# Kernel optimization log

Hardware: AMD Instinct MI355X
Metric: run time of the kernel (lower is better)

Reference implementation:

```python
import jax, jax.numpy as jnp
import numpy as np

NEG_SLOPE = 0.2  # PyG GATConv default negative_slope


def _gat_layer(x, src, dst, W, a_s, a_d, b, heads, ch):
    N = x.shape[0]
    h = (x @ W).reshape(N, heads, ch)                      # [N,H,C]
    al_s = jnp.sum(h * a_s[None], axis=-1)                 # [N,H]
    al_d = jnp.sum(h * a_d[None], axis=-1)                 # [N,H]
    e = jax.nn.leaky_relu(al_s[src] + al_d[dst], NEG_SLOPE)  # [E,H]
    m = jax.ops.segment_max(e, dst, num_segments=N)        # segment-softmax (stable)
    ex = jnp.exp(e - jax.lax.stop_gradient(m)[dst])
    denom = jax.ops.segment_sum(ex, dst, num_segments=N)
    alpha = ex / (denom[dst] + 1e-16)                      # [E,H]
    msg = h[src] * alpha[..., None]                        # [E,H,C]
    out = jax.ops.segment_sum(msg, dst, num_segments=N)    # [N,H,C]
    return out.reshape(N, heads * ch) + b


def _add_self_loops(edge_index, N):
    loop = jnp.arange(N, dtype=edge_index.dtype)
    src = jnp.concatenate([edge_index[0], loop])
    dst = jnp.concatenate([edge_index[1], loop])
    return src, dst


def gat_forward(x, edge_index, batch, W1, a_src1, a_dst1, b1, W2, a_src2, a_dst2, b2, W3, a_src3, a_dst3, b3, num_graphs=512):
    N = x.shape[0]
    src, dst = _add_self_loops(edge_index, N)
    x = jax.nn.relu(_gat_layer(x, src, dst, W1, a_src1, a_dst1, b1, 4, 64))
    x = jax.nn.relu(_gat_layer(x, src, dst, W2, a_src2, a_dst2, b2, 4, 64))
    x = _gat_layer(x, src, dst, W3, a_src3, a_dst3, b3, 1, 32)
    # global_mean_pool
    sums = jax.ops.segment_sum(x, batch, num_segments=num_graphs)
    cnt = jax.ops.segment_sum(jnp.ones((N,), x.dtype), batch, num_segments=num_graphs)
    return sums / jnp.maximum(cnt, 1.0)[:, None]


def setup_inputs() -> dict:
    key = jax.random.key(0)
    ks = jax.random.split(key, 16)
    N, E, G = 50000, 800000, 512
    IN, HID, H, OUT = 775, 64, 4, 32
    s = 0.05
    return {
        "x": jax.random.normal(ks[0], (N, IN), jnp.float32),
        "edge_index": jax.random.randint(ks[1], (2, E), 0, N, jnp.int32),
        "batch": jnp.sort(jax.random.randint(ks[2], (N,), 0, G, jnp.int32)),
        "W1": jax.random.normal(ks[3], (IN, H * HID), jnp.float32) * s,
        "a_src1": jax.random.normal(ks[4], (H, HID), jnp.float32) * s,
        "a_dst1": jax.random.normal(ks[5], (H, HID), jnp.float32) * s,
        "b1": jnp.zeros((H * HID,), jnp.float32),
        "W2": jax.random.normal(ks[6], (H * HID, H * HID), jnp.float32) * s,
        "a_src2": jax.random.normal(ks[7], (H, HID), jnp.float32) * s,
        "a_dst2": jax.random.normal(ks[8], (H, HID), jnp.float32) * s,
        "b2": jnp.zeros((H * HID,), jnp.float32),
        "W3": jax.random.normal(ks[9], (H * HID, OUT), jnp.float32) * s,
        "a_src3": jax.random.normal(ks[10], (1, OUT), jnp.float32) * s,
        "a_dst3": jax.random.normal(ks[11], (1, OUT), jnp.float32) * s,
        "b3": jnp.zeros((OUT,), jnp.float32),
    }


def reference(x, edge_index, batch, W1, a_src1, a_dst1, b1, W2, a_src2, a_dst2, b2, W3, a_src3, a_dst3, b3):
    return gat_forward(x, edge_index, batch, W1, a_src1, a_dst1, b1, W2, a_src2, a_dst2, b2, W3, a_src3, a_dst3, b3)
```

## Files before the change

### kernel.cpp

```cpp
#include <hip/hip_runtime.h>
#include <hip/hip_bf16.h>

typedef unsigned short u16;
typedef __attribute__((ext_vector_type(4))) unsigned short u16x4;
typedef __attribute__((ext_vector_type(8))) unsigned short u16x8;
typedef __attribute__((ext_vector_type(8))) short bf16x8;
typedef __attribute__((ext_vector_type(4))) float f32x4;

__device__ __forceinline__ u16 f2bs(float f) {
    union { float f; unsigned int u; } x; x.f = f;
    unsigned int r = x.u + 0x7FFFu + ((x.u >> 16) & 1u);
    return (u16)(r >> 16);
}
__device__ __forceinline__ float bs2f(u16 u) {
    union { unsigned int u; float f; } x; x.u = ((unsigned int)u) << 16; return x.f;
}
__device__ __forceinline__ float lrelu(float e) { return e >= 0.f ? e : 0.2f * e; }

__global__ void deg_kernel(const int* __restrict__ dst, int* __restrict__ deg, int E) {
    int i = blockIdx.x * 256 + threadIdx.x;
    if (i < E) atomicAdd(&deg[dst[i]], 1);
}

__global__ __launch_bounds__(1024) void scan_local(const int* __restrict__ deg,
        int* __restrict__ ptr, int* __restrict__ bsum, int N) {
    __shared__ int wsum[16];
    const int t = threadIdx.x, i = blockIdx.x * 1024 + t;
    const int lane = t & 63, w = t >> 6;
    int v = (i < N) ? deg[i] : 0;
    int x = v;
    #pragma unroll
    for (int off = 1; off < 64; off <<= 1) { int y = __shfl_up(x, off); if (lane >= off) x += y; }
    if (lane == 63) wsum[w] = x;
    __syncthreads();
    if (w == 0) {
        int s = (lane < 16) ? wsum[lane] : 0;
        #pragma unroll
        for (int off = 1; off < 16; off <<= 1) { int y = __shfl_up(s, off); if (lane >= off) s += y; }
        if (lane < 16) wsum[lane] = s;
    }
    __syncthreads();
    int incl = x + (w > 0 ? wsum[w - 1] : 0);
    if (i < N) ptr[i + 1] = incl;
    if (t == 0) bsum[blockIdx.x] = wsum[15];
}

__global__ __launch_bounds__(64) void scan_carry(int* __restrict__ bsum, int nb) {
    int t = threadIdx.x;
    int v = (t < nb) ? bsum[t] : 0;
    int x = v;
    #pragma unroll
    for (int off = 1; off < 64; off <<= 1) { int y = __shfl_up(x, off); if (t >= off) x += y; }
    if (t < nb) bsum[t] = x - v;
}

__global__ __launch_bounds__(1024) void scan_final(const int* __restrict__ deg,
        int* __restrict__ ptr, int* __restrict__ cur, const int* __restrict__ bsum, int N) {
    int i = blockIdx.x * 1024 + threadIdx.x;
    if (i == 0) ptr[0] = 0;
    if (i < N) {
        int p = ptr[i + 1] + bsum[blockIdx.x];
        ptr[i + 1] = p;
        cur[i] = p - deg[i];
    }
}

__global__ void fill_kernel(const int* __restrict__ src, const int* __restrict__ dst,
        int* __restrict__ cur, int* __restrict__ csr, int E) {
    int i = blockIdx.x * 256 + threadIdx.x;
    if (i < E) { int p = atomicAdd(&cur[dst[i]], 1); csr[p] = src[i]; }
}

__global__ void bounds_kernel(const int* __restrict__ batch, int* __restrict__ gstart,
        int N, int G) {
    int i = blockIdx.x * 256 + threadIdx.x;
    if (i > N) return;
    if (i == 0) {
        int b0 = batch[0];
        for (int g = 0; g <= b0; g++) gstart[g] = 0;
    } else if (i == N) {
        int bl = batch[N - 1];
        for (int g = bl + 1; g <= G; g++) gstart[g] = N;
    } else {
        int b = batch[i], bp = batch[i - 1];
        for (int g = bp + 1; g <= b; g++) gstart[g] = i;
    }
}

__global__ void transpose_w(const float* __restrict__ W, u16* __restrict__ Wt,
        int K, int Nn, int KT) {
    int idx = blockIdx.x * 256 + threadIdx.x;
    if (idx >= Nn * KT) return;
    int n = idx / KT, k = idx - n * KT;
    Wt[(size_t)n * KT + k] = (k < K) ? f2bs(W[(size_t)k * Nn + n]) : (u16)0;
}

__global__ __launch_bounds__(256) void conv_x(const float* __restrict__ x,
        u16* __restrict__ xbf, int N) {
    const int idx = blockIdx.x * 256 + threadIdx.x;
    if (idx >= N * 200) return;
    const int r = idx / 200;
    const int k4 = (idx - r * 200) * 4;
    const float* row = x + (size_t)r * 775;
    u16x4 o;
    #pragma unroll
    for (int u = 0; u < 4; u++) {
        const int k = k4 + u;
        o[u] = (k < 775) ? f2bs(row[k]) : (u16)0;
    }
    *(u16x4*)&xbf[(size_t)r * 800 + k4] = o;
}

template<bool AFP32>
__global__ __launch_bounds__(256) void gemm128(
        const void* __restrict__ Av, int lda, int M, int K,
        const u16* __restrict__ B, int ldb,
        u16* __restrict__ C, int ldc) {
    const float* Af = (const float*)Av;
    const u16*   Au = (const u16*)Av;
    __shared__ u16 Alds[128][40];
    __shared__ u16 Blds[128][40];
    const int t = threadIdx.x;
    const int row0 = blockIdx.x * 128, col0 = blockIdx.y * 128;
    const int wid = t >> 6, lane = t & 63;
    const int wm = wid >> 1, wn = wid & 1;
    const int quad = lane >> 4, l16 = lane & 15;

    f32x4 acc[4][4];
    f32x4 z = {0.f, 0.f, 0.f, 0.f};
    #pragma unroll
    for (int i = 0; i < 4; i++)
        #pragma unroll
        for (int j = 0; j < 4; j++) acc[i][j] = z;

    const int kTiles = (K + 31) >> 5;
    for (int kt = 0; kt < kTiles; ++kt) {
        const int k0 = kt << 5;
        #pragma unroll
        for (int c = 0; c < 2; c++) {
            int ch = t + c * 256;
            int r = ch >> 2, cp = (ch & 3) * 8;
            int gr = row0 + r;
            u16x8 v = {0,0,0,0,0,0,0,0};
            if (AFP32) {
                #pragma unroll
                for (int u = 0; u < 8; u++) {
                    int k = k0 + cp + u;
                    v[u] = (gr < M && k < K) ? f2bs(Af[(size_t)gr * lda + k]) : (u16)0;
                }
            } else {
                if (gr < M) v = *(const u16x8*)(Au + (size_t)gr * lda + k0 + cp);
            }
            *(u16x8*)&Alds[r][cp] = v;
        }
        #pragma unroll
        for (int c = 0; c < 2; c++) {
            int ch = t + c * 256;
            int r = ch >> 2, cp = (ch & 3) * 8;
            *(u16x8*)&Blds[r][cp] = *(const u16x8*)(B + (size_t)(col0 + r) * ldb + k0 + cp);
        }
        __syncthreads();
        bf16x8 af[4], bfr[4];
        #pragma unroll
        for (int it = 0; it < 4; it++) af[it] = *(const bf16x8*)&Alds[wm * 64 + it * 16 + l16][quad * 8];
        #pragma unroll
        for (int jt = 0; jt < 4; jt++) bfr[jt] = *(const bf16x8*)&Blds[wn * 64 + jt * 16 + l16][quad * 8];
        #pragma unroll
        for (int it = 0; it < 4; it++)
            #pragma unroll
            for (int jt = 0; jt < 4; jt++)
                acc[it][jt] = __builtin_amdgcn_mfma_f32_16x16x32_bf16(af[it], bfr[jt], acc[it][jt], 0, 0, 0);
        __syncthreads();
    }
    #pragma unroll
    for (int it = 0; it < 4; it++) {
        int gr0 = row0 + wm * 64 + it * 16 + quad * 4;
        #pragma unroll
        for (int jt = 0; jt < 4; jt++) {
            int gc = col0 + wn * 64 + jt * 16 + l16;
            #pragma unroll
            for (int r = 0; r < 4; r++) {
                int gr = gr0 + r;
                if (gr < M) C[(size_t)gr * ldc + gc] = f2bs(acc[it][jt][r]);
            }
        }
    }
}

__global__ __launch_bounds__(256) void gemm32(
        const u16* __restrict__ A, int lda, int M, int K,
        const u16* __restrict__ B, int ldb, float* __restrict__ C) {
    __shared__ u16 Alds[128][40];
    __shared__ u16 Blds[32][40];
    const int t = threadIdx.x;
    const int row0 = blockIdx.x * 128;
    const int wid = t >> 6, lane = t & 63;
    const int quad = lane >> 4, l16 = lane & 15;
    f32x4 acc[2][2];
    f32x4 z = {0.f, 0.f, 0.f, 0.f};
    acc[0][0] = z; acc[0][1] = z; acc[1][0] = z; acc[1][1] = z;
    const int kTiles = K >> 5;
    for (int kt = 0; kt < kTiles; ++kt) {
        const int k0 = kt << 5;
        #pragma unroll
        for (int c = 0; c < 2; c++) {
            int ch = t + c * 256;
            int r = ch >> 2, cp = (ch & 3) * 8;
            int gr = row0 + r;
            u16x8 v = {0,0,0,0,0,0,0,0};
            if (gr < M) v = *(const u16x8*)(A + (size_t)gr * lda + k0 + cp);
            *(u16x8*)&Alds[r][cp] = v;
        }
        if (t < 128) {
            int r = t >> 2, cp = (t & 3) * 8;
            *(u16x8*)&Blds[r][cp] = *(const u16x8*)(B + (size_t)r * ldb + k0 + cp);
        }
        __syncthreads();
        bf16x8 af[2], bfr[2];
        #pragma unroll
        for (int it = 0; it < 2; it++) af[it] = *(const bf16x8*)&Alds[wid * 32 + it * 16 + l16][quad * 8];
        #pragma unroll
        for (int jt = 0; jt < 2; jt++) bfr[jt] = *(const bf16x8*)&Blds[jt * 16 + l16][quad * 8];
        #pragma unroll
        for (int it = 0; it < 2; it++)
            #pragma unroll
            for (int jt = 0; jt < 2; jt++)
                acc[it][jt] = __builtin_amdgcn_mfma_f32_16x16x32_bf16(af[it], bfr[jt], acc[it][jt], 0, 0, 0);
        __syncthreads();
    }
    #pragma unroll
    for (int it = 0; it < 2; it++) {
        int gr0 = row0 + wid * 32 + it * 16 + quad * 4;
        #pragma unroll
        for (int jt = 0; jt < 2; jt++) {
            int gc = jt * 16 + l16;
            #pragma unroll
            for (int r = 0; r < 4; r++) {
                int gr = gr0 + r;
                if (gr < M) C[(size_t)gr * 32 + gc] = acc[it][jt][r];
            }
        }
    }
}

__global__ __launch_bounds__(256) void al_kernel(const u16* __restrict__ h,
        const float* __restrict__ a_s, const float* __restrict__ a_d,
        float* __restrict__ als, float* __restrict__ ald, int N) {
    const int t = threadIdx.x, wid = t >> 6, lane = t & 63;
    const f32x4 as4 = *(const f32x4*)&a_s[lane * 4];
    const f32x4 ad4 = *(const f32x4*)&a_d[lane * 4];
    #pragma unroll
    for (int u = 0; u < 2; u++) {
        const int n = blockIdx.x * 8 + wid * 2 + u;
        if (n >= N) return;
        const u16x4 hv = *(const u16x4*)&h[(size_t)n * 256 + lane * 4];
        float ps = 0.f, pd = 0.f;
        #pragma unroll
        for (int c = 0; c < 4; c++) {
            const float f = bs2f(hv[c]);
            ps = fmaf(f, as4[c], ps);
            pd = fmaf(f, ad4[c], pd);
        }
        #pragma unroll
        for (int off = 8; off >= 1; off >>= 1) {
            ps += __shfl_xor(ps, off, 16);
            pd += __shfl_xor(pd, off, 16);
        }
        if ((lane & 15) == 0) {
            als[n * 4 + (lane >> 4)] = ps;
            ald[n * 4 + (lane >> 4)] = pd;
        }
    }
}

__global__ __launch_bounds__(256) void al3_kernel(const float* __restrict__ h3,
        const float* __restrict__ a_s, const float* __restrict__ a_d,
        float* __restrict__ als, float* __restrict__ ald, int N) {
    int t = threadIdx.x, wid = t >> 6, lane = t & 63;
    int c = lane & 31, half = lane >> 5;
    float as = a_s[c], ad = a_d[c];
    int n = blockIdx.x * 8 + wid * 2 + half;
    if (n >= N) return;
    float hv = h3[(size_t)n * 32 + c];
    float ps = hv * as, pd = hv * ad;
    for (int off = 16; off >= 1; off >>= 1) { ps += __shfl_down(ps, off, 32); pd += __shfl_down(pd, off, 32); }
    if (c == 0) { als[n] = ps; ald[n] = pd; }
}

__global__ __launch_bounds__(256) void agg_kernel(const u16* __restrict__ hbuf,
        const float* __restrict__ als, const float* __restrict__ ald,
        const int* __restrict__ ptr, const int* __restrict__ csr,
        const float* __restrict__ bias, u16* __restrict__ act, int N) {
    __shared__ float al_lds[4][64][4];
    __shared__ int   s_lds[4][64];
    const int t = threadIdx.x, wid = t >> 6, lane = t & 63;
    const int i = blockIdx.x * 4 + wid;
    if (i >= N) return;
    const int start = ptr[i], end = ptr[i + 1];
    const int deg = end - start;
    const int col8 = lane & 31;
    const int half = lane >> 5;
    const int head8 = col8 >> 3;

    const f32x4 aldv = *(const f32x4*)&ald[(size_t)i * 4];
    const f32x4 alsv = *(const f32x4*)&als[(size_t)i * 4];
    f32x4 eself;
    #pragma unroll
    for (int hh = 0; hh < 4; hh++) eself[hh] = lrelu(alsv[hh] + aldv[hh]);

    float acc[8];
    f32x4 mx, inv;

    if (deg <= 64) {
        int sreg = 0;
        f32x4 ev;
        #pragma unroll
        for (int hh = 0; hh < 4; hh++) ev[hh] = -1e30f;
        if (lane < deg) {
            sreg = csr[start + lane];
            const f32x4 a = *(const f32x4*)&als[(size_t)sreg * 4];
            #pragma unroll
            for (int hh = 0; hh < 4; hh++) ev[hh] = lrelu(a[hh] + aldv[hh]);
        }
        #pragma unroll
        for (int hh = 0; hh < 4; hh++) mx[hh] = fmaxf(eself[hh], ev[hh]);
        #pragma unroll
        for (int off = 32; off >= 1; off >>= 1) {
            #pragma unroll
            for (int hh = 0; hh < 4; hh++) mx[hh] = fmaxf(mx[hh], __shfl_xor(mx[hh], off));
        }
        f32x4 sm, av;
        #pragma unroll
        for (int hh = 0; hh < 4; hh++) {
            av[hh] = (lane < deg) ? expf(ev[hh] - mx[hh]) : 0.f;
            sm[hh] = av[hh] + ((lane == 0) ? expf(eself[hh] - mx[hh]) : 0.f);
        }
        #pragma unroll
        for (int off = 32; off >= 1; off >>= 1) {
            #pragma unroll
            for (int hh = 0; hh < 4; hh++) sm[hh] += __shfl_xor(sm[hh], off);
        }
        #pragma unroll
        for (int hh = 0; hh < 4; hh++) inv[hh] = 1.f / (sm[hh] + 1e-16f);
        #pragma unroll
        for (int hh = 0; hh < 4; hh++) av[hh] *= inv[hh];
        *(f32x4*)&al_lds[wid][lane][0] = av;
        s_lds[wid][lane] = sreg;

        const u16x8 hrs = *(const u16x8*)&hbuf[(size_t)i * 256 + col8 * 8];
        const float aself = expf(eself[head8] - mx[head8]) * inv[head8];
        #pragma unroll
        for (int c = 0; c < 8; c++) acc[c] = (half == 0) ? aself * bs2f(hrs[c]) : 0.f;

        int k = half;
        for (; k + 6 < deg; k += 8) {
            const int s0 = s_lds[wid][k],     s1 = s_lds[wid][k + 2];
            const int s2 = s_lds[wid][k + 4], s3 = s_lds[wid][k + 6];
            const float a0 = al_lds[wid][k][head8],     a1 = al_lds[wid][k + 2][head8];
            const float a2 = al_lds[wid][k + 4][head8], a3 = al_lds[wid][k + 6][head8];
            const u16x8 h0 = *(const u16x8*)&hbuf[(size_t)s0 * 256 + col8 * 8];
            const u16x8 h1 = *(const u16x8*)&hbuf[(size_t)s1 * 256 + col8 * 8];
            const u16x8 h2 = *(const u16x8*)&hbuf[(size_t)s2 * 256 + col8 * 8];
            const u16x8 h3v = *(const u16x8*)&hbuf[(size_t)s3 * 256 + col8 * 8];
            #pragma unroll
            for (int c = 0; c < 8; c++) {
                acc[c] = fmaf(a0, bs2f(h0[c]), acc[c]);
                acc[c] = fmaf(a1, bs2f(h1[c]), acc[c]);
                acc[c] = fmaf(a2, bs2f(h2[c]), acc[c]);
                acc[c] = fmaf(a3, bs2f(h3v[c]), acc[c]);
            }
        }
        for (; k < deg; k += 2) {
            const int s = s_lds[wid][k];
            const float a = al_lds[wid][k][head8];
            const u16x8 hr = *(const u16x8*)&hbuf[(size_t)s * 256 + col8 * 8];
            #pragma unroll
            for (int c = 0; c < 8; c++) acc[c] = fmaf(a, bs2f(hr[c]), acc[c]);
        }
    } else {
        mx = eself;
        for (int j = start + lane; j < end; j += 64) {
            int s = csr[j];
            const f32x4 a = *(const f32x4*)&als[(size_t)s * 4];
            #pragma unroll
            for (int hh = 0; hh < 4; hh++) mx[hh] = fmaxf(mx[hh], lrelu(a[hh] + aldv[hh]));
        }
        #pragma unroll
        for (int off = 32; off >= 1; off >>= 1) {
            #pragma unroll
            for (int hh = 0; hh < 4; hh++) mx[hh] = fmaxf(mx[hh], __shfl_xor(mx[hh], off));
        }
        f32x4 sm;
        #pragma unroll
        for (int hh = 0; hh < 4; hh++) sm[hh] = (lane == 0) ? expf(eself[hh] - mx[hh]) : 0.f;
        for (int j = start + lane; j < end; j += 64) {
            int s = csr[j];
            const f32x4 a = *(const f32x4*)&als[(size_t)s * 4];
            #pragma unroll
            for (int hh = 0; hh < 4; hh++) sm[hh] += expf(lrelu(a[hh] + aldv[hh]) - mx[hh]);
        }
        #pragma unroll
        for (int off = 32; off >= 1; off >>= 1) {
            #pragma unroll
            for (int hh = 0; hh < 4; hh++) sm[hh] += __shfl_xor(sm[hh], off);
        }
        #pragma unroll
        for (int hh = 0; hh < 4; hh++) inv[hh] = 1.f / (sm[hh] + 1e-16f);

        const u16x8 hrs = *(const u16x8*)&hbuf[(size_t)i * 256 + col8 * 8];
        const float aself = expf(eself[head8] - mx[head8]) * inv[head8];
        #pragma unroll
        for (int c = 0; c < 8; c++) acc[c] = (half == 0) ? aself * bs2f(hrs[c]) : 0.f;

        for (int base = start; base < end; base += 64) {
            const int n64 = min(64, end - base);
            const int j = base + lane;
            int sreg = 0;
            if (j < end) {
                sreg = csr[j];
                const f32x4 a = *(const f32x4*)&als[(size_t)sreg * 4];
                f32x4 alpha;
                #pragma unroll
                for (int hh = 0; hh < 4; hh++)
                    alpha[hh] = expf(lrelu(a[hh] + aldv[hh]) - mx[hh]) * inv[hh];
                *(f32x4*)&al_lds[wid][lane][0] = alpha;
            }
            s_lds[wid][lane] = sreg;
            for (int k = half; k < n64; k += 2) {
                const int s = s_lds[wid][k];
                const float a = al_lds[wid][k][head8];
                const u16x8 hr = *(const u16x8*)&hbuf[(size_t)s * 256 + col8 * 8];
                #pragma unroll
                for (int c = 0; c < 8; c++) acc[c] = fmaf(a, bs2f(hr[c]), acc[c]);
            }
        }
    }

    #pragma unroll
    for (int c = 0; c < 8; c++) acc[c] += __shfl_down(acc[c], 32);
    if (half == 0) {
        const f32x4 bv0 = *(const f32x4*)&bias[col8 * 8];
        const f32x4 bv1 = *(const f32x4*)&bias[col8 * 8 + 4];
        u16x8 o;
        #pragma unroll
        for (int c = 0; c < 4; c++) o[c] = f2bs(fmaxf(acc[c] + bv0[c], 0.f));
        #pragma unroll
        for (int c = 4; c < 8; c++) o[c] = f2bs(fmaxf(acc[c] + bv1[c - 4], 0.f));
        *(u16x8*)&act[(size_t)i * 256 + col8 * 8] = o;
    }
}

__global__ __launch_bounds__(256) void agg3_kernel(const float* __restrict__ h3,
        const float* __restrict__ als, const float* __restrict__ ald,
        const int* __restrict__ ptr, const int* __restrict__ csr,
        const float* __restrict__ bias, float* __restrict__ out_n, int N) {
    __shared__ float a_lds[4][64];
    __shared__ int   s_lds3[4][64];
    const int t = threadIdx.x, wid = t >> 6, lane = t & 63;
    const int col = lane & 31, half = lane >> 5;
    const int i = blockIdx.x * 4 + wid;
    if (i >= N) return;
    const int start = ptr[i], end = ptr[i + 1];
    const int deg = end - start;
    const float aldv = ald[i];
    const float e0 = lrelu(als[i] + aldv);
    float acc = 0.f;

    if (deg <= 64) {
        int sreg = 0; float ev = -1e30f;
        if (lane < deg) { sreg = csr[start + lane]; ev = lrelu(als[sreg] + aldv); }
        float mx = fmaxf(e0, ev);
        #pragma unroll
        for (int off = 32; off >= 1; off >>= 1) mx = fmaxf(mx, __shfl_xor(mx, off));
        float ex = (lane < deg) ? expf(ev - mx) : 0.f;
        float sm = ex + ((lane == 0) ? expf(e0 - mx) : 0.f);
        #pragma unroll
        for (int off = 32; off >= 1; off >>= 1) sm += __shfl_xor(sm, off);
        const float inv = 1.f / (sm + 1e-16f);
        a_lds[wid][lane] = ex * inv;
        s_lds3[wid][lane] = sreg;
        if (half == 0) acc = expf(e0 - mx) * inv * h3[(size_t)i * 32 + col];

        int k = half;
        for (; k + 6 < deg; k += 8) {
            const int s0 = s_lds3[wid][k],     s1 = s_lds3[wid][k + 2];
            const int s2 = s_lds3[wid][k + 4], s3 = s_lds3[wid][k + 6];
            const float a0 = a_lds[wid][k],     a1 = a_lds[wid][k + 2];
            const float a2 = a_lds[wid][k + 4], a3 = a_lds[wid][k + 6];
            const float v0 = h3[(size_t)s0 * 32 + col];
            const float v1 = h3[(size_t)s1 * 32 + col];
            const float v2 = h3[(size_t)s2 * 32 + col];
            const float v3 = h3[(size_t)s3 * 32 + col];
            acc = fmaf(a0, v0, acc); acc = fmaf(a1, v1, acc);
            acc = fmaf(a2, v2, acc); acc = fmaf(a3, v3, acc);
        }
        for (; k < deg; k += 2)
            acc = fmaf(a_lds[wid][k], h3[(size_t)s_lds3[wid][k] * 32 + col], acc);
    } else {
        float mx = e0;
        for (int j = start + lane; j < end; j += 64)
            mx = fmaxf(mx, lrelu(als[csr[j]] + aldv));
        #pragma unroll
        for (int off = 32; off >= 1; off >>= 1) mx = fmaxf(mx, __shfl_xor(mx, off));
        float sm = (lane == 0) ? expf(e0 - mx) : 0.f;
        for (int j = start + lane; j < end; j += 64)
            sm += expf(lrelu(als[csr[j]] + aldv) - mx);
        #pragma unroll
        for (int off = 32; off >= 1; off >>= 1) sm += __shfl_xor(sm, off);
        const float inv = 1.f / (sm + 1e-16f);
        if (half == 0) acc = expf(e0 - mx) * inv * h3[(size_t)i * 32 + col];
        for (int base = start; base < end; base += 64) {
            const int n64 = min(64, end - base);
            const int j = base + lane;
            int sreg = 0; float av = 0.f;
            if (j < end) {
                sreg = csr[j];
                av = expf(lrelu(als[sreg] + aldv) - mx) * inv;
            }
            a_lds[wid][lane] = av;
            s_lds3[wid][lane] = sreg;
            for (int k = half; k < n64; k += 2)
                acc = fmaf(a_lds[wid][k], h3[(size_t)s_lds3[wid][k] * 32 + col], acc);
        }
    }

    acc += __shfl_down(acc, 32);
    if (half == 0)
        out_n[(size_t)i * 32 + col] = acc + bias[col];
}

__global__ __launch_bounds__(256) void pool_kernel(const float* __restrict__ out_n,
        const int* __restrict__ gstart, float* __restrict__ out, int G) {
    const int t = threadIdx.x, wid = t >> 6, lane = t & 63;
    const int col = lane & 31, half = lane >> 5;
    const int g = blockIdx.x * 4 + wid;
    if (g >= G) return;
    const int s = gstart[g], e = gstart[g + 1];
    float acc = 0.f;
    int r = s + half;
    for (; r + 6 < e; r += 8) {
        acc += out_n[(size_t)r * 32 + col];
        acc += out_n[(size_t)(r + 2) * 32 + col];
        acc += out_n[(size_t)(r + 4) * 32 + col];
        acc += out_n[(size_t)(r + 6) * 32 + col];
    }
    for (; r < e; r += 2) acc += out_n[(size_t)r * 32 + col];
    acc += __shfl_down(acc, 32);
    if (half == 0)
        out[g * 32 + col] = acc / fmaxf((float)(e - s), 1.f);
}

extern "C" void kernel_launch(void* const* d_in, const int* in_sizes, int n_in,
                              void* d_out, int out_size, void* d_ws, size_t ws_size,
                              hipStream_t stream) {
    const int N = 50000, E = 800000, G = 512;
    const float* x    = (const float*)d_in[0];
    const int*   ei   = (const int*)d_in[1];
    const int*   batch= (const int*)d_in[2];
    const float* W1   = (const float*)d_in[3];
    const float* as1  = (const float*)d_in[4];
    const float* ad1  = (const float*)d_in[5];
    const float* b1   = (const float*)d_in[6];
    const float* W2   = (const float*)d_in[7];
    const float* as2  = (const float*)d_in[8];
    const float* ad2  = (const float*)d_in[9];
    const float* b2   = (const float*)d_in[10];
    const float* W3   = (const float*)d_in[11];
    const float* as3  = (const float*)d_in[12];
    const float* ad3  = (const float*)d_in[13];
    const float* b3   = (const float*)d_in[14];
    const int* esrc = ei;
    const int* edst = ei + E;

    char* base = (char*)d_ws; size_t off = 0;
    auto alloc = [&](size_t bytes) -> void* {
        void* p = base + off; off = (off + bytes + 255) & ~(size_t)255; return p;
    };
    u16*   hbuf = (u16*)  alloc((size_t)N * 256 * 2);
    u16*   act  = (u16*)  alloc((size_t)N * 256 * 2);
    float* h3   = (float*)alloc((size_t)N * 32 * 4);
    float* als  = (float*)alloc((size_t)N * 4 * 4);
    float* ald  = (float*)alloc((size_t)N * 4 * 4);
    int*   deg  = (int*)  alloc((size_t)N * 4);
    int*   ptr  = (int*)  alloc((size_t)(N + 1) * 4);
    int*   cur  = (int*)  alloc((size_t)N * 4);
    int*   csr  = (int*)  alloc((size_t)E * 4);
    u16*   Wt   = (u16*)  alloc((size_t)256 * 800 * 2);
    int*   bsum = (int*)  alloc((size_t)64 * 4);
    float* out_n= (float*)alloc((size_t)N * 32 * 4);
    int*   gstart=(int*)  alloc((size_t)(G + 1) * 4);
    u16*   xbf  = (u16*)  alloc((size_t)N * 800 * 2);
    const bool use_xbf = (off <= ws_size);

    hipMemsetAsync(deg, 0, (size_t)N * 4, stream);

    const int nb = (N + 1023) / 1024;
    deg_kernel<<<(E + 255) / 256, 256, 0, stream>>>(edst, deg, E);
    scan_local<<<nb, 1024, 0, stream>>>(deg, ptr, bsum, N);
    scan_carry<<<1, 64, 0, stream>>>(bsum, nb);
    scan_final<<<nb, 1024, 0, stream>>>(deg, ptr, cur, bsum, N);
    fill_kernel<<<(E + 255) / 256, 256, 0, stream>>>(esrc, edst, cur, csr, E);
    bounds_kernel<<<(N + 256) / 256, 256, 0, stream>>>(batch, gstart, N, G);

    dim3 g128((N + 127) / 128, 2);
    const int aggGrid = (N + 3) / 4;
    transpose_w<<<(256 * 800 + 255) / 256, 256, 0, stream>>>(W1, Wt, 775, 256, 800);
    if (use_xbf) {
        conv_x<<<(N * 200 + 255) / 256, 256, 0, stream>>>(x, xbf, N);
        gemm128<false><<<g128, 256, 0, stream>>>(xbf, 800, N, 775, Wt, 800, hbuf, 256);
    } else {
        gemm128<true><<<g128, 256, 0, stream>>>(x, 775, N, 775, Wt, 800, hbuf, 256);
    }
    al_kernel<<<(N + 7) / 8, 256, 0, stream>>>(hbuf, as1, ad1, als, ald, N);
    agg_kernel<<<aggGrid, 256, 0, stream>>>(hbuf, als, ald, ptr, csr, b1, act, N);
    transpose_w<<<(256 * 256 + 255) / 256, 256, 0, stream>>>(W2, Wt, 256, 256, 256);
    gemm128<false><<<g128, 256, 0, stream>>>(act, 256, N, 256, Wt, 256, hbuf, 256);
    al_kernel<<<(N + 7) / 8, 256, 0, stream>>>(hbuf, as2, ad2, als, ald, N);
    agg_kernel<<<aggGrid, 256, 0, stream>>>(hbuf, als, ald, ptr, csr, b2, act, N);
    transpose_w<<<(32 * 256 + 255) / 256, 256, 0, stream>>>(W3, Wt, 256, 32, 256);
    gemm32<<<(N + 127) / 128, 256, 0, stream>>>(act, 256, N, 256, Wt, 256, h3);
    al3_kernel<<<(N + 7) / 8, 256, 0, stream>>>(h3, as3, ad3, als, ald, N);
    agg3_kernel<<<aggGrid, 256, 0, stream>>>(h3, als, ald, ptr, csr, b3, out_n, N);
    pool_kernel<<<(G + 3) / 4, 256, 0, stream>>>(out_n, gstart, (float*)d_out, G);
}
```

Baseline: 639.7 us.

## Widen GEMM tile to full 256 columns and fuse fp32-to-bf16 conversion into A load

```diff
diff --git a/kernel.cpp b/kernel.cpp
--- a/kernel.cpp
+++ b/kernel.cpp
@@ -95,45 +95,29 @@
     Wt[(size_t)n * KT + k] = (k < K) ? f2bs(W[(size_t)k * Nn + n]) : (u16)0;
 }
 
-__global__ __launch_bounds__(256) void conv_x(const float* __restrict__ x,
-        u16* __restrict__ xbf, int N) {
-    const int idx = blockIdx.x * 256 + threadIdx.x;
-    if (idx >= N * 200) return;
-    const int r = idx / 200;
-    const int k4 = (idx - r * 200) * 4;
-    const float* row = x + (size_t)r * 775;
-    u16x4 o;
-    #pragma unroll
-    for (int u = 0; u < 4; u++) {
-        const int k = k4 + u;
-        o[u] = (k < 775) ? f2bs(row[k]) : (u16)0;
-    }
-    *(u16x4*)&xbf[(size_t)r * 800 + k4] = o;
-}
-
 template<bool AFP32>
-__global__ __launch_bounds__(256) void gemm128(
-        const void* __restrict__ Av, int lda, int M, int K,
+__global__ __launch_bounds__(256) void gemm256(
+        const void* __restrict__ Av, int lda, int M, int K, int KT,
         const u16* __restrict__ B, int ldb,
         u16* __restrict__ C, int ldc) {
     const float* Af = (const float*)Av;
     const u16*   Au = (const u16*)Av;
     __shared__ u16 Alds[128][40];
-    __shared__ u16 Blds[128][40];
+    __shared__ u16 Blds[256][40];
     const int t = threadIdx.x;
-    const int row0 = blockIdx.x * 128, col0 = blockIdx.y * 128;
+    const int row0 = blockIdx.x * 128;
     const int wid = t >> 6, lane = t & 63;
     const int wm = wid >> 1, wn = wid & 1;
     const int quad = lane >> 4, l16 = lane & 15;
 
-    f32x4 acc[4][4];
+    f32x4 acc[4][8];
     f32x4 z = {0.f, 0.f, 0.f, 0.f};
     #pragma unroll
     for (int i = 0; i < 4; i++)
         #pragma unroll
-        for (int j = 0; j < 4; j++) acc[i][j] = z;
-
-    const int kTiles = (K + 31) >> 5;
+        for (int j = 0; j < 8; j++) acc[i][j] = z;
+
+    const int kTiles = KT >> 5;
     for (int kt = 0; kt < kTiles; ++kt) {
         const int k0 = kt << 5;
         #pragma unroll
@@ -143,10 +127,18 @@
             int gr = row0 + r;
             u16x8 v = {0,0,0,0,0,0,0,0};
             if (AFP32) {
-                #pragma unroll
-                for (int u = 0; u < 8; u++) {
-                    int k = k0 + cp + u;
-                    v[u] = (gr < M && k < K) ? f2bs(Af[(size_t)gr * lda + k]) : (u16)0;
+                if (gr < M) {
+                    const float* ap = Af + (size_t)gr * lda + k0 + cp;
+                    if (k0 + cp + 8 <= K) {
+                        #pragma unroll
+                        for (int u = 0; u < 8; u++) v[u] = f2bs(ap[u]);
+                    } else {
+                        #pragma unroll
+                        for (int u = 0; u < 8; u++) {
+                            int k = k0 + cp + u;
+                            v[u] = (k < K) ? f2bs(ap[u]) : (u16)0;
+                        }
+                    }
                 }
             } else {
                 if (gr < M) v = *(const u16x8*)(Au + (size_t)gr * lda + k0 + cp);
@@ -154,30 +146,30 @@
             *(u16x8*)&Alds[r][cp] = v;
         }
         #pragma unroll
-        for (int c = 0; c < 2; c++) {
+        for (int c = 0; c < 4; c++) {
             int ch = t + c * 256;
             int r = ch >> 2, cp = (ch & 3) * 8;
-            *(u16x8*)&Blds[r][cp] = *(const u16x8*)(B + (size_t)(col0 + r) * ldb + k0 + cp);
+            *(u16x8*)&Blds[r][cp] = *(const u16x8*)(B + (size_t)r * ldb + k0 + cp);
         }
         __syncthreads();
-        bf16x8 af[4], bfr[4];
+        bf16x8 af[4];
         #pragma unroll
         for (int it = 0; it < 4; it++) af[it] = *(const bf16x8*)&Alds[wm * 64 + it * 16 + l16][quad * 8];
         #pragma unroll
-        for (int jt = 0; jt < 4; jt++) bfr[jt] = *(const bf16x8*)&Blds[wn * 64 + jt * 16 + l16][quad * 8];
-        #pragma unroll
-        for (int it = 0; it < 4; it++)
-            #pragma unroll
-            for (int jt = 0; jt < 4; jt++)
-                acc[it][jt] = __builtin_amdgcn_mfma_f32_16x16x32_bf16(af[it], bfr[jt], acc[it][jt], 0, 0, 0);
+        for (int jt = 0; jt < 8; jt++) {
+            const bf16x8 bfr = *(const bf16x8*)&Blds[wn * 128 + jt * 16 + l16][quad * 8];
+            #pragma unroll
+            for (int it = 0; it < 4; it++)
+                acc[it][jt] = __builtin_amdgcn_mfma_f32_16x16x32_bf16(af[it], bfr, acc[it][jt], 0, 0, 0);
+        }
         __syncthreads();
     }
     #pragma unroll
     for (int it = 0; it < 4; it++) {
         int gr0 = row0 + wm * 64 + it * 16 + quad * 4;
         #pragma unroll
-        for (int jt = 0; jt < 4; jt++) {
-            int gc = col0 + wn * 64 + jt * 16 + l16;
+        for (int jt = 0; jt < 8; jt++) {
+            int gc = wn * 128 + jt * 16 + l16;
             #pragma unroll
             for (int r = 0; r < 4; r++) {
                 int gr = gr0 + r;
@@ -589,8 +581,6 @@
     int*   bsum = (int*)  alloc((size_t)64 * 4);
     float* out_n= (float*)alloc((size_t)N * 32 * 4);
     int*   gstart=(int*)  alloc((size_t)(G + 1) * 4);
-    u16*   xbf  = (u16*)  alloc((size_t)N * 800 * 2);
-    const bool use_xbf = (off <= ws_size);
 
     hipMemsetAsync(deg, 0, (size_t)N * 4, stream);
 
@@ -602,19 +592,14 @@
     fill_kernel<<<(E + 255) / 256, 256, 0, stream>>>(esrc, edst, cur, csr, E);
     bounds_kernel<<<(N + 256) / 256, 256, 0, stream>>>(batch, gstart, N, G);
 
-    dim3 g128((N + 127) / 128, 2);
+    const int gemmGrid = (N + 127) / 128;
     const int aggGrid = (N + 3) / 4;
     transpose_w<<<(256 * 800 + 255) / 256, 256, 0, stream>>>(W1, Wt, 775, 256, 800);
-    if (use_xbf) {
-        conv_x<<<(N * 200 + 255) / 256, 256, 0, stream>>>(x, xbf, N);
-        gemm128<false><<<g128, 256, 0, stream>>>(xbf, 800, N, 775, Wt, 800, hbuf, 256);
-    } else {
-        gemm128<true><<<g128, 256, 0, stream>>>(x, 775, N, 775, Wt, 800, hbuf, 256);
-    }
+    gemm256<true><<<gemmGrid, 256, 0, stream>>>(x, 775, N, 775, 800, Wt, 800, hbuf, 256);
     al_kernel<<<(N + 7) / 8, 256, 0, stream>>>(hbuf, as1, ad1, als, ald, N);
     agg_kernel<<<aggGrid, 256, 0, stream>>>(hbuf, als, ald, ptr, csr, b1, act, N);
     transpose_w<<<(256 * 256 + 255) / 256, 256, 0, stream>>>(W2, Wt, 256, 256, 256);
-    gemm128<false><<<g128, 256, 0, stream>>>(act, 256, N, 256, Wt, 256, hbuf, 256);
+    gemm256<false><<<gemmGrid, 256, 0, stream>>>(act, 256, N, 256, 256, Wt, 256, hbuf, 256);
     al_kernel<<<(N + 7) / 8, 256, 0, stream>>>(hbuf, as2, ad2, als, ald, N);
     agg_kernel<<<aggGrid, 256, 0, stream>>>(hbuf, als, ald, ptr, csr, b2, act, N);
     transpose_w<<<(32 * 256 + 255) / 256, 256, 0, stream>>>(W3, Wt, 256, 32, 256);
```

New measurement: 643.3 us. No clear change (+0.6%).

## Load GEMM tiles directly into LDS with XOR-swizzled layout

Applied to the files above, without the earlier changes.

```diff
diff --git a/kernel.cpp b/kernel.cpp
--- a/kernel.cpp
+++ b/kernel.cpp
@@ -16,6 +16,12 @@
     union { unsigned int u; float f; } x; x.u = ((unsigned int)u) << 16; return x.f;
 }
 __device__ __forceinline__ float lrelu(float e) { return e >= 0.f ? e : 0.2f * e; }
+
+__device__ __forceinline__ void glds16(const void* g, void* l) {
+    __builtin_amdgcn_global_load_lds(
+        (const __attribute__((address_space(1))) unsigned int*)g,
+        (__attribute__((address_space(3))) unsigned int*)l, 16, 0, 0);
+}
 
 __global__ void deg_kernel(const int* __restrict__ dst, int* __restrict__ deg, int E) {
     int i = blockIdx.x * 256 + threadIdx.x;
@@ -111,17 +117,15 @@
     *(u16x4*)&xbf[(size_t)r * 800 + k4] = o;
 }
 
-template<bool AFP32>
-__global__ __launch_bounds__(256) void gemm128(
-        const void* __restrict__ Av, int lda, int M, int K,
+__global__ __launch_bounds__(256) void gemm_glds(
+        const u16* __restrict__ A, int lda, int M, int K,
         const u16* __restrict__ B, int ldb,
         u16* __restrict__ C, int ldc) {
-    const float* Af = (const float*)Av;
-    const u16*   Au = (const u16*)Av;
-    __shared__ u16 Alds[128][40];
-    __shared__ u16 Blds[128][40];
+    __shared__ u16 Alds[128][32];
+    __shared__ u16 Blds[128][32];
     const int t = threadIdx.x;
-    const int row0 = blockIdx.x * 128, col0 = blockIdx.y * 128;
+    const int col0 = blockIdx.x * 128;
+    const int row0 = blockIdx.y * 128;
     const int wid = t >> 6, lane = t & 63;
     const int wm = wid >> 1, wn = wid & 1;
     const int quad = lane >> 4, l16 = lane & 15;
@@ -133,38 +137,30 @@
         #pragma unroll
         for (int j = 0; j < 4; j++) acc[i][j] = z;
 
-    const int kTiles = (K + 31) >> 5;
+    const int trb = wid * 32 + (lane >> 2);
+    const int kTiles = K >> 5;
     for (int kt = 0; kt < kTiles; ++kt) {
         const int k0 = kt << 5;
         #pragma unroll
         for (int c = 0; c < 2; c++) {
-            int ch = t + c * 256;
-            int r = ch >> 2, cp = (ch & 3) * 8;
-            int gr = row0 + r;
-            u16x8 v = {0,0,0,0,0,0,0,0};
-            if (AFP32) {
-                #pragma unroll
-                for (int u = 0; u < 8; u++) {
-                    int k = k0 + cp + u;
-                    v[u] = (gr < M && k < K) ? f2bs(Af[(size_t)gr * lda + k]) : (u16)0;
-                }
-            } else {
-                if (gr < M) v = *(const u16x8*)(Au + (size_t)gr * lda + k0 + cp);
-            }
-            *(u16x8*)&Alds[r][cp] = v;
-        }
-        #pragma unroll
-        for (int c = 0; c < 2; c++) {
-            int ch = t + c * 256;
-            int r = ch >> 2, cp = (ch & 3) * 8;
-            *(u16x8*)&Blds[r][cp] = *(const u16x8*)(B + (size_t)(col0 + r) * ldb + k0 + cp);
+            const int tr = trb + c * 16;
+            const int ks = ((lane & 3) ^ ((tr >> 1) & 3)) * 8;
+            int gra = row0 + tr; if (gra > M - 1) gra = M - 1;
+            glds16(A + (size_t)gra * lda + k0 + ks, &Alds[wid * 32 + c * 16][0]);
+            glds16(B + (size_t)(col0 + tr) * ldb + k0 + ks, &Blds[wid * 32 + c * 16][0]);
         }
         __syncthreads();
         bf16x8 af[4], bfr[4];
         #pragma unroll
-        for (int it = 0; it < 4; it++) af[it] = *(const bf16x8*)&Alds[wm * 64 + it * 16 + l16][quad * 8];
-        #pragma unroll
-        for (int jt = 0; jt < 4; jt++) bfr[jt] = *(const bf16x8*)&Blds[wn * 64 + jt * 16 + l16][quad * 8];
+        for (int it = 0; it < 4; it++) {
+            const int r = wm * 64 + it * 16 + l16;
+            af[it] = *(const bf16x8*)&Alds[r][(quad ^ ((r >> 1) & 3)) * 8];
+        }
+        #pragma unroll
+        for (int jt = 0; jt < 4; jt++) {
+            const int r = wn * 64 + jt * 16 + l16;
+            bfr[jt] = *(const bf16x8*)&Blds[r][(quad ^ ((r >> 1) & 3)) * 8];
+        }
         #pragma unroll
         for (int it = 0; it < 4; it++)
             #pragma unroll
@@ -590,7 +586,6 @@
     float* out_n= (float*)alloc((size_t)N * 32 * 4);
     int*   gstart=(int*)  alloc((size_t)(G + 1) * 4);
     u16*   xbf  = (u16*)  alloc((size_t)N * 800 * 2);
-    const bool use_xbf = (off <= ws_size);
 
     hipMemsetAsync(deg, 0, (size_t)N * 4, stream);
 
@@ -602,19 +597,15 @@
     fill_kernel<<<(E + 255) / 256, 256, 0, stream>>>(esrc, edst, cur, csr, E);
     bounds_kernel<<<(N + 256) / 256, 256, 0, stream>>>(batch, gstart, N, G);
 
-    dim3 g128((N + 127) / 128, 2);
+    dim3 gemmGrid(2, (N + 127) / 128);
     const int aggGrid = (N + 3) / 4;
     transpose_w<<<(256 * 800 + 255) / 256, 256, 0, stream>>>(W1, Wt, 775, 256, 800);
-    if (use_xbf) {
-        conv_x<<<(N * 200 + 255) / 256, 256, 0, stream>>>(x, xbf, N);
-        gemm128<false><<<g128, 256, 0, stream>>>(xbf, 800, N, 775, Wt, 800, hbuf, 256);
-    } else {
-        gemm128<true><<<g128, 256, 0, stream>>>(x, 775, N, 775, Wt, 800, hbuf, 256);
-    }
+    conv_x<<<(N * 200 + 255) / 256, 256, 0, stream>>>(x, xbf, N);
+    gemm_glds<<<gemmGrid, 256, 0, stream>>>(xbf, 800, N, 800, Wt, 800, hbuf, 256);
     al_kernel<<<(N + 7) / 8, 256, 0, stream>>>(hbuf, as1, ad1, als, ald, N);
     agg_kernel<<<aggGrid, 256, 0, stream>>>(hbuf, als, ald, ptr, csr, b1, act, N);
     transpose_w<<<(256 * 256 + 255) / 256, 256, 0, stream>>>(W2, Wt, 256, 256, 256);
-    gemm128<false><<<g128, 256, 0, stream>>>(act, 256, N, 256, Wt, 256, hbuf, 256);
+    gemm_glds<<<gemmGrid, 256, 0, stream>>>(act, 256, N, 256, Wt, 256, hbuf, 256);
     al_kernel<<<(N + 7) / 8, 256, 0, stream>>>(hbuf, as2, ad2, als, ald, N);
     agg_kernel<<<aggGrid, 256, 0, stream>>>(hbuf, als, ald, ptr, csr, b2, act, N);
     transpose_w<<<(32 * 256 + 255) / 256, 256, 0, stream>>>(W3, Wt, 256, 32, 256);
```

Result: faster. 625.4 us (-2.2%).
